# Kernel tuning notes

Measured on AMD Instinct MI355X. Metric: run time of the kernel, lower is better.

The kernel has to match this reference:

```python
import jax, jax.numpy as jnp
import numpy as np

C, H, O, T, B = 15, 256, 512, 60, 1024


def setup_inputs() -> dict:
    key = jax.random.key(0)
    ks = jax.random.split(key, 8)
    s = 1.0 / np.sqrt(H)
    return {
        "x": jax.random.normal(ks[0], (B, H), dtype=jnp.float32),
        "cam": jax.random.randint(ks[1], (B,), 0, C, dtype=jnp.int32),
        "W_ih": jax.random.uniform(ks[2], (C, 3 * H, H), jnp.float32, -s, s),
        "W_hh": jax.random.uniform(ks[3], (C, 3 * H, H), jnp.float32, -s, s),
        "b_ih": jax.random.uniform(ks[4], (C, 3 * H), jnp.float32, -s, s),
        "b_hh": jax.random.uniform(ks[5], (C, 3 * H), jnp.float32, -s, s),
        "Wc": jax.random.uniform(ks[6], (C, O, H), jnp.float32, -s, s),
        "bc": jax.random.uniform(ks[7], (C, O), jnp.float32, -s, s),
    }


def reference(x, cam, W_ih, W_hh, b_ih, b_hh, Wc, bc):
    # Gather per-sample (per-camera) parameters once.
    Wi = W_ih[cam]          # [B, 3H, H]
    Wh = W_hh[cam]          # [B, 3H, H]
    bi = b_ih[cam]          # [B, 3H]
    bh = b_hh[cam]          # [B, 3H]
    Wcs = Wc[cam]           # [B, O, H]
    bcs = bc[cam]           # [B, O]

    # Input is constant across timesteps -> input gate preactivations computed once.
    gi = jnp.einsum('bh,bgh->bg', x, Wi) + bi   # [B, 3H]
    gi_r, gi_z, gi_n = jnp.split(gi, 3, axis=1)

    h0 = jnp.zeros_like(x)  # [B, H]

    def step(h, _):
        gh = jnp.einsum('bh,bgh->bg', h, Wh) + bh
        gh_r, gh_z, gh_n = jnp.split(gh, 3, axis=1)
        r = jax.nn.sigmoid(gi_r + gh_r)
        z = jax.nn.sigmoid(gi_z + gh_z)
        n = jnp.tanh(gi_n + r * gh_n)
        h_new = (1.0 - z) * n + z * h
        out = jax.nn.sigmoid(jnp.einsum('bh,boh->bo', h_new, Wcs) + bcs)  # [B, O]
        return h_new, out

    _, outs = jax.lax.scan(step, h0, None, length=T)  # [T, B, O]
    return jnp.transpose(outs, (1, 2, 0))             # [B, O, T]
```

## Files before the change

kernel.cpp:

```cpp
#include <hip/hip_runtime.h>
#include <hip/hip_fp16.h>

#define C_    15
#define H_    256
#define O_    512
#define T_    60
#define B_    1024
#define G3H_  768
#define TS    16
#define MAXG  12
#define NSLOT 96
#define NU    80
#define TCH   10

typedef __attribute__((ext_vector_type(8))) short bf16x8;
typedef __attribute__((ext_vector_type(4))) float f32x4;

__device__ __forceinline__ unsigned short f2bf(float f) {
    union { float f; unsigned u; } v; v.f = f;
    return (unsigned short)((v.u + 0x7FFFu + ((v.u >> 16) & 1u)) >> 16);
}
__device__ __forceinline__ float sigf(float x) { return 1.f / (1.f + __expf(-x)); }

__global__ __launch_bounds__(256) void sort_kernel(const int* __restrict__ cam,
    int* __restrict__ order, int* __restrict__ tcam, int* __restrict__ toff,
    int* __restrict__ tcnt)
{
    __shared__ int cnt[C_], start[C_], fill[C_];
    int tid = threadIdx.x;
    if (tid < C_) cnt[tid] = 0;
    if (tid < NSLOT) { tcam[tid] = -1; toff[tid] = 0; tcnt[tid] = 0; }
    __syncthreads();
    for (int b = tid; b < B_; b += 256) atomicAdd(&cnt[cam[b]], 1);
    __syncthreads();
    if (tid == 0) {
        int run = 0;
        for (int c = 0; c < C_; ++c) { start[c] = run; fill[c] = run; run += cnt[c]; }
    }
    __syncthreads();
    for (int b = tid; b < B_; b += 256) {
        int pos = atomicAdd(&fill[cam[b]], 1);
        order[pos] = b;
    }
    __syncthreads();
    if (tid == 0) {
        int gcnt[8] = {0,0,0,0,0,0,0,0};
        for (int c = 0; c < C_; ++c) gcnt[c & 7] += (cnt[c] + TS - 1) / TS;
        int maxg = 0;
        for (int g = 0; g < 8; ++g) maxg = max(maxg, gcnt[g]);
        if (maxg <= MAXG) {
            for (int g = 0; g < 8; ++g) {
                int k = 0;
                for (int c = g; c < C_; c += 8)
                    for (int r = 0; r < cnt[c]; r += TS) {
                        int slot = g + 8 * k;
                        tcam[slot] = c; toff[slot] = start[c] + r;
                        tcnt[slot] = min(TS, cnt[c] - r); ++k;
                    }
            }
        } else {
            int ti = 0;
            for (int c = 0; c < C_; ++c)
                for (int r = 0; r < cnt[c]; r += TS) {
                    tcam[ti] = c; toff[ti] = start[c] + r;
                    tcnt[ti] = min(TS, cnt[c] - r); ++ti;
                }
        }
    }
}

__global__ __launch_bounds__(256) void cvt_kernel(const float* __restrict__ src,
    unsigned short* __restrict__ dst, int n4)
{
    int i = blockIdx.x * 256 + threadIdx.x;
    if (i < n4) {
        float4 v = ((const float4*)src)[i];
        unsigned p0 = (unsigned)f2bf(v.x) | ((unsigned)f2bf(v.y) << 16);
        unsigned p1 = (unsigned)f2bf(v.z) | ((unsigned)f2bf(v.w) << 16);
        ((uint2*)dst)[i] = make_uint2(p0, p1);
    }
}

__global__ __launch_bounds__(64) void pack_kernel(
    const float* __restrict__ Whh, const float* __restrict__ Wc,
    unsigned short* __restrict__ Wpack)
{
    int cu = blockIdx.x;
    int c = cu / NU, u = cu - c * NU;
    int lane = threadIdx.x, q = lane >> 4, l16 = lane & 15;
    const float* src = (u < 48)
        ? &Whh[((size_t)c * G3H_ + u * 16 + l16) * H_]
        : &Wc[((size_t)c * O_ + (u - 48) * 16 + l16) * H_];
    unsigned short* dst = Wpack + ((size_t)cu * 8) * 512 + lane * 8;
#pragma unroll
    for (int kk = 0; kk < 8; ++kk) {
        float4 v0 = *(const float4*)&src[kk * 32 + q * 8];
        float4 v1 = *(const float4*)&src[kk * 32 + q * 8 + 4];
        unsigned short* d = dst + kk * 512;
        d[0] = f2bf(v0.x); d[1] = f2bf(v0.y); d[2] = f2bf(v0.z); d[3] = f2bf(v0.w);
        d[4] = f2bf(v1.x); d[5] = f2bf(v1.y); d[6] = f2bf(v1.z); d[7] = f2bf(v1.w);
    }
}

__global__ __launch_bounds__(384) void gi_mfma(
    const float* __restrict__ x, const unsigned short* __restrict__ Wih_b,
    const float* __restrict__ bih, const float* __restrict__ bhh,
    const int* __restrict__ order, const int* __restrict__ tcam,
    const int* __restrict__ toff, const int* __restrict__ tcnt,
    float* __restrict__ gi)
{
    int c = tcam[blockIdx.x]; if (c < 0) return;
    int cnt = tcnt[blockIdx.x], off = toff[blockIdx.x];
    int tid = threadIdx.x;
    __shared__ unsigned short hbfs[TS * 264];
    __shared__ int ord16[TS];
    if (tid < TS) ord16[tid] = (tid < cnt) ? order[off + tid] : 0;
    for (int idx = tid; idx < TS * 64; idx += 384) {
        int m = idx >> 6, c4 = idx & 63;
        float4 v = make_float4(0.f, 0.f, 0.f, 0.f);
        if (m < cnt) v = *(const float4*)&x[(size_t)order[off + m] * H_ + (c4 << 2)];
        unsigned p0 = (unsigned)f2bf(v.x) | ((unsigned)f2bf(v.y) << 16);
        unsigned p1 = (unsigned)f2bf(v.z) | ((unsigned)f2bf(v.w) << 16);
        *(uint2*)&hbfs[m * 264 + (c4 << 2)] = make_uint2(p0, p1);
    }
    __syncthreads();
    int w = tid >> 6, lane = tid & 63, q = lane >> 4, l16 = lane & 15;
    f32x4 acc[2][4];
#pragma unroll
    for (int i = 0; i < 2; ++i)
#pragma unroll
        for (int nt = 0; nt < 4; ++nt) acc[i][nt] = (f32x4){0.f, 0.f, 0.f, 0.f};
    const unsigned short* bp[2];
#pragma unroll
    for (int i = 0; i < 2; ++i)
        bp[i] = Wih_b + ((size_t)c * G3H_ + (2 * w + i) * 64 + l16) * H_;
    const unsigned short* ap = &hbfs[l16 * 264 + q * 8];
#pragma unroll 2
    for (int kk = 0; kk < 8; ++kk) {
        bf16x8 a = *(const bf16x8*)(ap + kk * 32);
#pragma unroll
        for (int i = 0; i < 2; ++i)
#pragma unroll
            for (int nt = 0; nt < 4; ++nt) {
                bf16x8 b = *(const bf16x8*)(bp[i] + (size_t)nt * 16 * H_ + kk * 32 + q * 8);
                acc[i][nt] = __builtin_amdgcn_mfma_f32_16x16x32_bf16(a, b, acc[i][nt], 0, 0, 0);
            }
    }
#pragma unroll
    for (int i = 0; i < 2; ++i) {
        int u = 2 * w + i;
#pragma unroll
        for (int nt = 0; nt < 4; ++nt) {
            int col = u * 64 + nt * 16 + l16;
            float bias = bih[c * G3H_ + col] + (col < 2 * H_ ? bhh[c * G3H_ + col] : 0.f);
#pragma unroll
            for (int r = 0; r < 4; ++r) {
                int m = q * 4 + r;
                if (m < cnt) gi[(size_t)ord16[m] * G3H_ + col] = acc[i][nt][r] + bias;
            }
        }
    }
}

__global__ __launch_bounds__(512, 2) void persist_kernel(
    const unsigned short* __restrict__ Wpack, const float* __restrict__ bhh,
    const float* __restrict__ gi, const int* __restrict__ order,
    const int* __restrict__ tcam, const int* __restrict__ toff,
    const int* __restrict__ tcnt, unsigned short* __restrict__ htraj)
{
    int slot = blockIdx.x;
    int c = tcam[slot]; if (c < 0) return;
    int n = tcnt[slot], off = toff[slot];
    int tid = threadIdx.x, w = tid >> 6, lane = tid & 63, q = lane >> 4, l16 = lane & 15;

    __shared__ float gis[16][772];
    __shared__ float P[16][772];
    __shared__ float hfp[16][260];
    __shared__ unsigned short hbf[16][264];

    for (int i = tid; i < 16 * 772; i += 512) ((float*)P)[i] = 0.f;
    for (int i = tid; i < 16 * 260; i += 512) ((float*)hfp)[i] = 0.f;
    for (int i = tid; i < 16 * 264; i += 512) ((unsigned short*)hbf)[i] = 0;
    for (int idx = tid; idx < 16 * 192; idx += 512) {
        int m = idx / 192, c4 = idx - m * 192;
        float4 v = make_float4(0.f, 0.f, 0.f, 0.f);
        if (m < n) v = *(const float4*)&gi[(size_t)order[off + m] * G3H_ + (c4 << 2)];
        *(float4*)&gis[m][c4 << 2] = v;
    }

    bf16x8 wf[6][8];
    const unsigned short* wb = Wpack + ((size_t)c * NU + w * 6) * 8 * 512 + lane * 8;
#pragma unroll
    for (int ui = 0; ui < 6; ++ui)
#pragma unroll
        for (int kk = 0; kk < 8; ++kk)
            wf[ui][kk] = *(const bf16x8*)(wb + ((size_t)ui * 8 + kk) * 512);

    int ucol = tid & 255, mh = (tid >> 8) * 8;
    float bhn = bhh[c * G3H_ + 2 * H_ + ucol];
    __syncthreads();

    for (int s = 0; s < T_; ++s) {
        if (s > 0) {
            f32x4 acc[6];
#pragma unroll
            for (int ui = 0; ui < 6; ++ui) acc[ui] = (f32x4){0.f, 0.f, 0.f, 0.f};
#pragma unroll
            for (int kk = 0; kk < 8; ++kk) {
                bf16x8 a = *(const bf16x8*)&hbf[l16][kk * 32 + q * 8];
#pragma unroll
                for (int ui = 0; ui < 6; ++ui)
                    acc[ui] = __builtin_amdgcn_mfma_f32_16x16x32_bf16(a, wf[ui][kk], acc[ui], 0, 0, 0);
            }
#pragma unroll
            for (int ui = 0; ui < 6; ++ui) {
                int col = (w * 6 + ui) * 16 + l16;
#pragma unroll
                for (int r = 0; r < 4; ++r) P[q * 4 + r][col] = acc[ui][r];
            }
            __syncthreads();
        }
        unsigned short* hrow = htraj + (((size_t)s * NSLOT + slot) * 16) * 256;
#pragma unroll
        for (int i = 0; i < 8; ++i) {
            int m = mh + i;
            float rr = sigf(gis[m][ucol] + P[m][ucol]);
            float zz = sigf(gis[m][256 + ucol] + P[m][256 + ucol]);
            float pre = gis[m][512 + ucol] + rr * (P[m][512 + ucol] + bhn);
            float nn = 2.f * sigf(2.f * pre) - 1.f;
            float hnew = (1.f - zz) * nn + zz * hfp[m][ucol];
            hfp[m][ucol] = hnew;
            unsigned short hb = f2bf(hnew);
            hbf[m][ucol] = hb;
            hrow[m * 256 + ucol] = hb;
        }
        __syncthreads();
    }
}

__global__ __launch_bounds__(512, 2) void out_kernel(
    const unsigned short* __restrict__ Wpack, const float* __restrict__ bc,
    const unsigned short* __restrict__ htraj, const int* __restrict__ order,
    const int* __restrict__ tcam, const int* __restrict__ toff,
    const int* __restrict__ tcnt, unsigned short* __restrict__ outT,
    int direct, float* __restrict__ outp)
{
    int slot = blockIdx.x;
    int c = tcam[slot]; if (c < 0) return;
    int n = tcnt[slot], off = toff[slot];
    int tid = threadIdx.x, w = tid >> 6, lane = tid & 63, q = lane >> 4, l16 = lane & 15;
    __shared__ unsigned short hb[16][264];
    __shared__ int ord16[16];
    if (tid < 16) ord16[tid] = (tid < n) ? order[off + tid] : -1;

    bf16x8 wf[4][8];
    const unsigned short* wb = Wpack + ((size_t)c * NU + 48 + w * 4) * 8 * 512 + lane * 8;
#pragma unroll
    for (int ui = 0; ui < 4; ++ui)
#pragma unroll
        for (int kk = 0; kk < 8; ++kk)
            wf[ui][kk] = *(const bf16x8*)(wb + ((size_t)ui * 8 + kk) * 512);
    float bcr[4];
#pragma unroll
    for (int ui = 0; ui < 4; ++ui)
        bcr[ui] = bc[c * O_ + (w * 4 + ui) * 16 + l16];
    __syncthreads();

    for (int ti = 0; ti < TCH; ++ti) {
        int t = blockIdx.y * TCH + ti;
        {
            int m = tid >> 5, c8 = (tid & 31) * 8;
            uint4 v = *(const uint4*)&htraj[(((size_t)t * NSLOT + slot) * 16 + m) * 256 + c8];
            *(uint4*)&hb[m][c8] = v;
        }
        __syncthreads();
        f32x4 acc[4];
#pragma unroll
        for (int ui = 0; ui < 4; ++ui) acc[ui] = (f32x4){0.f, 0.f, 0.f, 0.f};
#pragma unroll
        for (int kk = 0; kk < 8; ++kk) {
            bf16x8 a = *(const bf16x8*)&hb[l16][kk * 32 + q * 8];
#pragma unroll
            for (int ui = 0; ui < 4; ++ui)
                acc[ui] = __builtin_amdgcn_mfma_f32_16x16x32_bf16(a, wf[ui][kk], acc[ui], 0, 0, 0);
        }
#pragma unroll
        for (int ui = 0; ui < 4; ++ui) {
            int o = (w * 4 + ui) * 16 + l16;
#pragma unroll
            for (int r = 0; r < 4; ++r) {
                int b = ord16[q * 4 + r];
                if (b >= 0) {
                    float val = sigf(acc[ui][r] + bcr[ui]);
                    if (direct) outp[((size_t)b * O_ + o) * T_ + t] = val;
                    else outT[((size_t)t * B_ + b) * O_ + o] =
                             __half_as_ushort(__float2half_rn(val));
                }
            }
        }
        __syncthreads();
    }
}

__global__ __launch_bounds__(256) void transpose_kernel(
    const unsigned short* __restrict__ outT, float* __restrict__ outp)
{
    int b = blockIdx.x, o0 = blockIdx.y * 64;
    __shared__ float ts[T_][65];
    int tid = threadIdx.x;
    for (int idx = tid; idx < T_ * 64; idx += 256) {
        int t = idx >> 6, o = idx & 63;
        ts[t][o] = __half2float(__ushort_as_half(outT[((size_t)t * B_ + b) * O_ + o0 + o]));
    }
    __syncthreads();
    for (int idx = tid; idx < 64 * T_; idx += 256) {
        int o = idx / T_, t = idx - o * T_;
        outp[((size_t)b * O_ + o0 + o) * T_ + t] = ts[t][o];
    }
}

extern "C" void kernel_launch(void* const* d_in, const int* in_sizes, int n_in,
                              void* d_out, int out_size, void* d_ws, size_t ws_size,
                              hipStream_t stream)
{
    const float* x   = (const float*)d_in[0];
    const int*   cam = (const int*)d_in[1];
    const float* Wih = (const float*)d_in[2];
    const float* Whh = (const float*)d_in[3];
    const float* bih = (const float*)d_in[4];
    const float* bhh = (const float*)d_in[5];
    const float* Wc  = (const float*)d_in[6];
    const float* bc  = (const float*)d_in[7];
    float* outp = (float*)d_out;

    char* w = (char*)d_ws;
    unsigned short* Wih_b = (unsigned short*)w; w += (size_t)C_ * G3H_ * H_ * 2;
    unsigned short* Wpack = (unsigned short*)w; w += (size_t)C_ * NU * 8 * 512 * 2;
    int* order = (int*)w; w += B_ * 4;
    int* tcam  = (int*)w; w += NSLOT * 4;
    int* toff  = (int*)w; w += NSLOT * 4;
    int* tcnt  = (int*)w; w += NSLOT * 4;
    float* gi  = (float*)w; w += (size_t)B_ * G3H_ * 4;
    unsigned short* htraj = (unsigned short*)w; w += (size_t)T_ * NSLOT * 16 * 256 * 2;
    unsigned short* outT = (unsigned short*)w;
    size_t need = (size_t)(w - (char*)d_ws) + (size_t)T_ * B_ * O_ * 2;
    int direct = (ws_size < need) ? 1 : 0;

    sort_kernel<<<1, 256, 0, stream>>>(cam, order, tcam, toff, tcnt);
    cvt_kernel<<<(C_ * G3H_ * H_ / 4 + 255) / 256, 256, 0, stream>>>(Wih, Wih_b, C_ * G3H_ * H_ / 4);
    pack_kernel<<<C_ * NU, 64, 0, stream>>>(Whh, Wc, Wpack);
    gi_mfma<<<NSLOT, 384, 0, stream>>>(x, Wih_b, bih, bhh, order, tcam, toff, tcnt, gi);
    persist_kernel<<<NSLOT, 512, 0, stream>>>(Wpack, bhh, gi, order, tcam, toff, tcnt, htraj);
    out_kernel<<<dim3(NSLOT, T_ / TCH), 512, 0, stream>>>(Wpack, bc, htraj, order, tcam,
                                                          toff, tcnt, outT, direct, outp);
    if (!direct)
        transpose_kernel<<<dim3(B_, O_ / 64), 256, 0, stream>>>(outT, outp);
}
```

Measured before the change: 503.0 us.

## Keep GRU gate math in MFMA registers and double-buffer hidden state

The recurrent step now runs the gate nonlinearities directly on the MFMA accumulator fragments. It remaps which weight tiles each wave owns so that the r, z and n gates for the same columns land in one wave's registers. This removes the shared-memory P buffer, the second barrier per timestep and the fp32 hidden state kept in LDS. The hidden state now lives in registers and the bf16 copy is double-buffered, so one barrier per step suffices. The gi buffer is also stored slot-major, so the persist kernel reads it without an indirection and keeps it transposed in LDS. The trade-off is more register pressure and scattered 2-byte stores to htraj.

Measured after the change: 449.2 us. -10.7%, faster.

```diff
diff --git a/kernel.cpp b/kernel.cpp
--- a/kernel.cpp
+++ b/kernel.cpp
@@ -113,8 +113,6 @@
     int cnt = tcnt[blockIdx.x], off = toff[blockIdx.x];
     int tid = threadIdx.x;
     __shared__ unsigned short hbfs[TS * 264];
-    __shared__ int ord16[TS];
-    if (tid < TS) ord16[tid] = (tid < cnt) ? order[off + tid] : 0;
     for (int idx = tid; idx < TS * 64; idx += 384) {
         int m = idx >> 6, c4 = idx & 63;
         float4 v = make_float4(0.f, 0.f, 0.f, 0.f);
@@ -156,7 +154,7 @@
 #pragma unroll
             for (int r = 0; r < 4; ++r) {
                 int m = q * 4 + r;
-                if (m < cnt) gi[(size_t)ord16[m] * G3H_ + col] = acc[i][nt][r] + bias;
+                gi[((size_t)(blockIdx.x * TS + m)) * G3H_ + col] = acc[i][nt][r] + bias;
             }
         }
     }
@@ -164,76 +162,77 @@
 
 __global__ __launch_bounds__(512, 2) void persist_kernel(
     const unsigned short* __restrict__ Wpack, const float* __restrict__ bhh,
-    const float* __restrict__ gi, const int* __restrict__ order,
-    const int* __restrict__ tcam, const int* __restrict__ toff,
-    const int* __restrict__ tcnt, unsigned short* __restrict__ htraj)
+    const float* __restrict__ gi, const int* __restrict__ tcam,
+    unsigned short* __restrict__ htraj)
 {
     int slot = blockIdx.x;
     int c = tcam[slot]; if (c < 0) return;
-    int n = tcnt[slot], off = toff[slot];
     int tid = threadIdx.x, w = tid >> 6, lane = tid & 63, q = lane >> 4, l16 = lane & 15;
 
-    __shared__ float gis[16][772];
-    __shared__ float P[16][772];
-    __shared__ float hfp[16][260];
-    __shared__ unsigned short hbf[16][264];
-
-    for (int i = tid; i < 16 * 772; i += 512) ((float*)P)[i] = 0.f;
-    for (int i = tid; i < 16 * 260; i += 512) ((float*)hfp)[i] = 0.f;
-    for (int i = tid; i < 16 * 264; i += 512) ((unsigned short*)hbf)[i] = 0;
-    for (int idx = tid; idx < 16 * 192; idx += 512) {
-        int m = idx / 192, c4 = idx - m * 192;
-        float4 v = make_float4(0.f, 0.f, 0.f, 0.f);
-        if (m < n) v = *(const float4*)&gi[(size_t)order[off + m] * G3H_ + (c4 << 2)];
-        *(float4*)&gis[m][c4 << 2] = v;
+    __shared__ float gisT[G3H_][20];
+    __shared__ unsigned short hbf[2][16][264];
+
+    for (int idx = tid; idx < TS * G3H_; idx += 512) {
+        int m = idx / G3H_, col = idx - m * G3H_;
+        gisT[col][m] = gi[((size_t)(slot * TS + m)) * G3H_ + col];
     }
 
     bf16x8 wf[6][8];
-    const unsigned short* wb = Wpack + ((size_t)c * NU + w * 6) * 8 * 512 + lane * 8;
-#pragma unroll
-    for (int ui = 0; ui < 6; ++ui)
-#pragma unroll
-        for (int kk = 0; kk < 8; ++kk)
-            wf[ui][kk] = *(const bf16x8*)(wb + ((size_t)ui * 8 + kk) * 512);
-
-    int ucol = tid & 255, mh = (tid >> 8) * 8;
-    float bhn = bhh[c * G3H_ + 2 * H_ + ucol];
-    __syncthreads();
-
+#pragma unroll
+    for (int ii = 0; ii < 3; ++ii)
+#pragma unroll
+        for (int jj = 0; jj < 2; ++jj)
+#pragma unroll
+            for (int kk = 0; kk < 8; ++kk)
+                wf[ii * 2 + jj][kk] = *(const bf16x8*)(
+                    Wpack + (((size_t)(c * NU + ii * 16 + w + 8 * jj)) * 8 + kk) * 512 + lane * 8);
+
+    float bhn[2], hreg[2][4];
+#pragma unroll
+    for (int i = 0; i < 2; ++i) {
+        int col = (w + 8 * i) * 16 + l16;
+        bhn[i] = bhh[c * G3H_ + 2 * H_ + col];
+#pragma unroll
+        for (int r = 0; r < 4; ++r) hreg[i][r] = 0.f;
+    }
+    unsigned short* hp = htraj + ((size_t)slot * TS + q * 4) * 256 + w * 16 + l16;
+    __syncthreads();
+
+#pragma unroll 2
     for (int s = 0; s < T_; ++s) {
+        int wbuf = s & 1, rbuf = wbuf ^ 1;
+        f32x4 acc[6];
+#pragma unroll
+        for (int ui = 0; ui < 6; ++ui) acc[ui] = (f32x4){0.f, 0.f, 0.f, 0.f};
         if (s > 0) {
-            f32x4 acc[6];
-#pragma unroll
-            for (int ui = 0; ui < 6; ++ui) acc[ui] = (f32x4){0.f, 0.f, 0.f, 0.f};
 #pragma unroll
             for (int kk = 0; kk < 8; ++kk) {
-                bf16x8 a = *(const bf16x8*)&hbf[l16][kk * 32 + q * 8];
+                bf16x8 a = *(const bf16x8*)&hbf[rbuf][l16][kk * 32 + q * 8];
 #pragma unroll
                 for (int ui = 0; ui < 6; ++ui)
                     acc[ui] = __builtin_amdgcn_mfma_f32_16x16x32_bf16(a, wf[ui][kk], acc[ui], 0, 0, 0);
             }
-#pragma unroll
-            for (int ui = 0; ui < 6; ++ui) {
-                int col = (w * 6 + ui) * 16 + l16;
-#pragma unroll
-                for (int r = 0; r < 4; ++r) P[q * 4 + r][col] = acc[ui][r];
-            }
-            __syncthreads();
-        }
-        unsigned short* hrow = htraj + (((size_t)s * NSLOT + slot) * 16) * 256;
-#pragma unroll
-        for (int i = 0; i < 8; ++i) {
-            int m = mh + i;
-            float rr = sigf(gis[m][ucol] + P[m][ucol]);
-            float zz = sigf(gis[m][256 + ucol] + P[m][256 + ucol]);
-            float pre = gis[m][512 + ucol] + rr * (P[m][512 + ucol] + bhn);
-            float nn = 2.f * sigf(2.f * pre) - 1.f;
-            float hnew = (1.f - zz) * nn + zz * hfp[m][ucol];
-            hfp[m][ucol] = hnew;
-            unsigned short hb = f2bf(hnew);
-            hbf[m][ucol] = hb;
-            hrow[m * 256 + ucol] = hb;
-        }
+        }
+#pragma unroll
+        for (int i = 0; i < 2; ++i) {
+            int col = (w + 8 * i) * 16 + l16;
+            f32x4 gr = *(const f32x4*)&gisT[col][q * 4];
+            f32x4 gz = *(const f32x4*)&gisT[H_ + col][q * 4];
+            f32x4 gn = *(const f32x4*)&gisT[2 * H_ + col][q * 4];
+#pragma unroll
+            for (int r = 0; r < 4; ++r) {
+                float rr = sigf(gr[r] + acc[i][r]);
+                float zz = sigf(gz[r] + acc[2 + i][r]);
+                float pre = gn[r] + rr * (acc[4 + i][r] + bhn[i]);
+                float nn = 2.f * sigf(2.f * pre) - 1.f;
+                float hn = (1.f - zz) * nn + zz * hreg[i][r];
+                hreg[i][r] = hn;
+                unsigned short hb = f2bf(hn);
+                hbf[wbuf][q * 4 + r][col] = hb;
+                hp[r * 256 + i * 128] = hb;
+            }
+        }
+        hp += (size_t)NSLOT * TS * 256;
         __syncthreads();
     }
 }
@@ -340,7 +339,7 @@
     int* tcam  = (int*)w; w += NSLOT * 4;
     int* toff  = (int*)w; w += NSLOT * 4;
     int* tcnt  = (int*)w; w += NSLOT * 4;
-    float* gi  = (float*)w; w += (size_t)B_ * G3H_ * 4;
+    float* gi  = (float*)w; w += (size_t)NSLOT * TS * G3H_ * 4;
     unsigned short* htraj = (unsigned short*)w; w += (size_t)T_ * NSLOT * 16 * 256 * 2;
     unsigned short* outT = (unsigned short*)w;
     size_t need = (size_t)(w - (char*)d_ws) + (size_t)T_ * B_ * O_ * 2;
@@ -350,7 +349,7 @@
     cvt_kernel<<<(C_ * G3H_ * H_ / 4 + 255) / 256, 256, 0, stream>>>(Wih, Wih_b, C_ * G3H_ * H_ / 4);
     pack_kernel<<<C_ * NU, 64, 0, stream>>>(Whh, Wc, Wpack);
     gi_mfma<<<NSLOT, 384, 0, stream>>>(x, Wih_b, bih, bhh, order, tcam, toff, tcnt, gi);
-    persist_kernel<<<NSLOT, 512, 0, stream>>>(Wpack, bhh, gi, order, tcam, toff, tcnt, htraj);
+    persist_kernel<<<NSLOT, 512, 0, stream>>>(Wpack, bhh, gi, tcam, htraj);
     out_kernel<<<dim3(NSLOT, T_ / TCH), 512, 0, stream>>>(Wpack, bc, htraj, order, tcam,
                                                           toff, tcnt, outT, direct, outp);
     if (!direct)
```
